# Kernel tuning notes

Hardware: AMD Instinct MI355X
Metric: run time of the kernel (lower is better)

## Reference

```python
import jax, jax.numpy as jnp
import numpy as np


def setup_inputs() -> dict:
    key = jax.random.key(0)
    ks = jax.random.split(key, 5)
    B, Lq, Lk, KD, E, VD = 2, 1024, 1024, 128, 128, 128
    return {
        "query": jax.random.normal(ks[0], (B, Lq, KD), dtype=jnp.float32),
        "key": jax.random.normal(ks[1], (B, Lk, KD), dtype=jnp.float32),
        "value": jax.random.normal(ks[2], (B, Lk, VD), dtype=jnp.float32),
        "vT": jax.random.normal(ks[3], (E,), dtype=jnp.float32) * (1.0 / np.sqrt(E)),
        "weight": jax.random.normal(ks[4], (E, 2 * KD), dtype=jnp.float32) * (1.0 / np.sqrt(2 * KD)),
    }


def reference(query, key, value, vT, weight):
    # Additive (Bahdanau) attention: score(i,j) = vT . tanh(W @ concat(q_i, k_j))
    kdim = query.shape[-1]
    Wq = weight[:, :kdim]   # [E, kdim] acts on query half of concat
    Wk = weight[:, kdim:]   # [E, kdim] acts on key half
    qp = jnp.einsum("bqd,ed->bqe", query, Wq)   # [B, Lq, E]
    kp = jnp.einsum("bkd,ed->bke", key, Wk)     # [B, Lk, E]
    # broadcast-add replaces the explicit concat+linear: [B, Lq, Lk, E]
    h = jnp.tanh(qp[:, :, None, :] + kp[:, None, :, :])
    scores = jnp.einsum("bqke,e->bqk", h, vT)    # [B, Lq, Lk]
    attn = jax.nn.softmax(scores, axis=-1)
    return jnp.einsum("bqk,bkv->bqv", attn, value)  # [B, Lq, Vd]
```

## Files before the change

### kernel.cpp

```cpp
#include <hip/hip_runtime.h>

#define CSC 2.88539008177792681f

typedef float v2f __attribute__((ext_vector_type(2)));

__device__ __forceinline__ float fast_exp2(float x) {
  return __builtin_amdgcn_exp2f(x);
}
__device__ __forceinline__ float fast_rcp(float x) {
  return __builtin_amdgcn_rcpf(x);
}
__device__ __forceinline__ v2f vfma(v2f a, v2f b, v2f c) {
  return __builtin_elementwise_fma(a, b, c);
}
__device__ __forceinline__ v2f vsplat(float s) {
  v2f r;
  r[0] = s;
  r[1] = s;
  return r;
}

__global__ __launch_bounds__(256) void proj_kernel(
    const float* __restrict__ query, const float* __restrict__ key,
    const float* __restrict__ weight, float* __restrict__ Eq,
    float* __restrict__ EkT) {
  __shared__ __align__(16) float rows[16][128];
  __shared__ __align__(16) float tile[16][128];
  int blk = blockIdx.x;
  bool isK = blk >= 128;
  const float* src = isK ? key : query;
  int woff = isK ? 128 : 0;
  int row0 = (isK ? blk - 128 : blk) * 16;
  int tid = threadIdx.x;
#pragma unroll
  for (int i = 0; i < 8; ++i) {
    int f = i * 256 + tid;
    rows[f >> 7][f & 127] = src[(size_t)row0 * 128 + f];
  }
  __syncthreads();
  int e = tid & 127;
  int rh = (tid >> 7) * 8;
  float acc[8];
#pragma unroll
  for (int i = 0; i < 8; ++i) acc[i] = 0.f;
  const float4* wrow =
      reinterpret_cast<const float4*>(weight + (size_t)e * 256 + woff);
#pragma unroll 4
  for (int d4 = 0; d4 < 32; ++d4) {
    float4 wv = wrow[d4];
#pragma unroll
    for (int i = 0; i < 8; ++i) {
      float4 rv = *reinterpret_cast<const float4*>(&rows[rh + i][d4 * 4]);
      acc[i] = fmaf(rv.x, wv.x, acc[i]);
      acc[i] = fmaf(rv.y, wv.y, acc[i]);
      acc[i] = fmaf(rv.z, wv.z, acc[i]);
      acc[i] = fmaf(rv.w, wv.w, acc[i]);
    }
  }
  if (!isK) {
#pragma unroll
    for (int i = 0; i < 8; ++i)
      Eq[(size_t)(row0 + rh + i) * 128 + e] = fast_exp2(CSC * acc[i]);
  } else {
#pragma unroll
    for (int i = 0; i < 8; ++i) tile[rh + i][e] = fast_exp2(CSC * acc[i]);
    __syncthreads();
    int eo = tid >> 1;
    int rseg = (tid & 1) * 8;
    float4 v0 = make_float4(tile[rseg + 0][eo], tile[rseg + 1][eo],
                            tile[rseg + 2][eo], tile[rseg + 3][eo]);
    float4 v1 = make_float4(tile[rseg + 4][eo], tile[rseg + 5][eo],
                            tile[rseg + 6][eo], tile[rseg + 7][eo]);
    float* dst = EkT + (size_t)eo * 2048 + row0 + rseg;
    *reinterpret_cast<float4*>(dst) = v0;
    *reinterpret_cast<float4*>(dst + 4) = v1;
  }
}

__device__ __forceinline__ void quad4(const float4 eq, const float4 vt, v2f ek0,
                                      v2f ek1, v2f ek2, v2f ek3, v2f& acc) {
  v2f one = vsplat(1.f);
  v2f A0 = vfma(vsplat(eq.x), ek0, one);
  v2f A1 = vfma(vsplat(eq.y), ek1, one);
  v2f A2 = vfma(vsplat(eq.z), ek2, one);
  v2f A3 = vfma(vsplat(eq.w), ek3, one);
  v2f P01 = A0 * A1;
  v2f P23 = A2 * A3;
  v2f t01 = vfma(vsplat(vt.x), A1, vsplat(vt.y) * A0);
  v2f t23 = vfma(vsplat(vt.z), A3, vsplat(vt.w) * A2);
  v2f num = vfma(t23, P01, t01 * P23);
  v2f den = P01 * P23;
  v2f r;
  r[0] = fast_rcp(den[0]);
  r[1] = fast_rcp(den[1]);
  acc = vfma(num, r, acc);
}

__global__ __launch_bounds__(1024, 4) void attn_kernel(
    const float* __restrict__ Eq, const float* __restrict__ EkT,
    const float* __restrict__ vT, const float* __restrict__ value,
    float* __restrict__ out) {
  __shared__ __align__(16) float sc[8][1024];
  __shared__ __align__(16) v2f pout[16][8][64];
  __shared__ float wsum[16][4];
  __shared__ float denom[8];

  int tid = threadIdx.x;
  int lane = tid & 63;
  int w = tid >> 6;
  int b = blockIdx.x >> 7;
  int q0 = (blockIdx.x & 127) * 8;
  int half = tid >> 9;
  int kp = tid & 511;
  int qh = half * 4;

  {
    const float* ekp = EkT + (size_t)b * 1024 + 2 * kp;
    const float* eqb = Eq + (size_t)(b * 1024 + q0 + qh) * 128;
    v2f acc[4];
#pragma unroll
    for (int q = 0; q < 4; ++q) acc[q] = vsplat(0.f);
#pragma unroll 2
    for (int e = 0; e < 128; e += 4) {
      v2f ek0 = *reinterpret_cast<const v2f*>(ekp + (size_t)(e + 0) * 2048);
      v2f ek1 = *reinterpret_cast<const v2f*>(ekp + (size_t)(e + 1) * 2048);
      v2f ek2 = *reinterpret_cast<const v2f*>(ekp + (size_t)(e + 2) * 2048);
      v2f ek3 = *reinterpret_cast<const v2f*>(ekp + (size_t)(e + 3) * 2048);
      float4 vt4 = *reinterpret_cast<const float4*>(vT + e);
#pragma unroll
      for (int q = 0; q < 4; ++q) {
        float4 eq4 =
            *reinterpret_cast<const float4*>(eqb + (size_t)q * 128 + e);
        quad4(eq4, vt4, ek0, ek1, ek2, ek3, acc[q]);
      }
    }
#pragma unroll
    for (int q = 0; q < 4; ++q) {
      v2f p;
      p[0] = fast_exp2(-CSC * acc[q][0]);
      p[1] = fast_exp2(-CSC * acc[q][1]);
      *reinterpret_cast<v2f*>(&sc[qh + q][2 * kp]) = p;
      float s = p[0] + p[1];
#pragma unroll
      for (int off = 32; off; off >>= 1) s += __shfl_xor(s, off);
      if (lane == 0) wsum[w][q] = s;
    }
  }
  __syncthreads();
  if (tid < 8) {
    int base = (tid >> 2) * 8;
    float s = 0.f;
#pragma unroll
    for (int ww = 0; ww < 8; ++ww) s += wsum[base + ww][tid & 3];
    denom[tid] = s;
  }

  {
    int kb = w * 64;
    v2f acc2[8];
#pragma unroll
    for (int q = 0; q < 8; ++q) acc2[q] = vsplat(0.f);
    const v2f* vp =
        reinterpret_cast<const v2f*>(value) + (size_t)b * 1024 * 64 + lane;
#pragma unroll 2
    for (int kk = 0; kk < 64; kk += 4) {
      v2f vv0 = vp[(size_t)(kb + kk + 0) * 64];
      v2f vv1 = vp[(size_t)(kb + kk + 1) * 64];
      v2f vv2 = vp[(size_t)(kb + kk + 2) * 64];
      v2f vv3 = vp[(size_t)(kb + kk + 3) * 64];
#pragma unroll
      for (int q = 0; q < 8; ++q) {
        float4 pp = *reinterpret_cast<const float4*>(&sc[q][kb + kk]);
        acc2[q] = vfma(vsplat(pp.x), vv0, acc2[q]);
        acc2[q] = vfma(vsplat(pp.y), vv1, acc2[q]);
        acc2[q] = vfma(vsplat(pp.z), vv2, acc2[q]);
        acc2[q] = vfma(vsplat(pp.w), vv3, acc2[q]);
      }
    }
#pragma unroll
    for (int q = 0; q < 8; ++q) pout[w][q][lane] = acc2[q];
  }
  __syncthreads();

  if (tid < 512) {
    int q = tid >> 6;
    v2f r = pout[0][q][lane];
#pragma unroll
    for (int ww = 1; ww < 16; ++ww) r = r + pout[ww][q][lane];
    float inv = fast_rcp(denom[q]);
    r[0] *= inv;
    r[1] *= inv;
    reinterpret_cast<v2f*>(out)[(size_t)(b * 1024 + q0 + q) * 64 + lane] = r;
  }
}

extern "C" void kernel_launch(void* const* d_in, const int* in_sizes, int n_in,
                              void* d_out, int out_size, void* d_ws,
                              size_t ws_size, hipStream_t stream) {
  const float* query = (const float*)d_in[0];
  const float* key = (const float*)d_in[1];
  const float* value = (const float*)d_in[2];
  const float* vT = (const float*)d_in[3];
  const float* weight = (const float*)d_in[4];
  float* out = (float*)d_out;
  float* Eq = (float*)d_ws;
  float* EkT = Eq + 2048 * 128;
  proj_kernel<<<256, 256, 0, stream>>>(query, key, weight, Eq, EkT);
  attn_kernel<<<256, 1024, 0, stream>>>(Eq, EkT, vT, value, out);
}
```

Baseline: 55.44 us.

## Store key projections in e4-interleaved layout and give each thread one key over eight queries

The proj kernel now writes the exponentiated key projections in a layout where four consecutive E-values of a key sit together as a float4, using a padded shared tile. The score loop has each thread handle one key and all eight queries with scalar math, replacing two keys times four queries with packed v2f math. This means one float4 load feeds eight queries and the query loads are warp-uniform. The final reduction now uses all 1024 threads, each writing one scalar output. The risk is losing packed-FMA throughput and raising register pressure from eight scalar accumulators.

```diff
diff --git a/kernel.cpp b/kernel.cpp
--- a/kernel.cpp
+++ b/kernel.cpp
@@ -23,9 +23,9 @@
 __global__ __launch_bounds__(256) void proj_kernel(
     const float* __restrict__ query, const float* __restrict__ key,
     const float* __restrict__ weight, float* __restrict__ Eq,
-    float* __restrict__ EkT) {
+    float* __restrict__ EkT4) {
   __shared__ __align__(16) float rows[16][128];
-  __shared__ __align__(16) float tile[16][128];
+  __shared__ __align__(16) float tile[16][132];
   int blk = blockIdx.x;
   bool isK = blk >= 128;
   const float* src = isK ? key : query;
@@ -65,44 +65,25 @@
 #pragma unroll
     for (int i = 0; i < 8; ++i) tile[rh + i][e] = fast_exp2(CSC * acc[i]);
     __syncthreads();
-    int eo = tid >> 1;
-    int rseg = (tid & 1) * 8;
-    float4 v0 = make_float4(tile[rseg + 0][eo], tile[rseg + 1][eo],
-                            tile[rseg + 2][eo], tile[rseg + 3][eo]);
-    float4 v1 = make_float4(tile[rseg + 4][eo], tile[rseg + 5][eo],
-                            tile[rseg + 6][eo], tile[rseg + 7][eo]);
-    float* dst = EkT + (size_t)eo * 2048 + row0 + rseg;
-    *reinterpret_cast<float4*>(dst) = v0;
-    *reinterpret_cast<float4*>(dst + 4) = v1;
+    int kk = tid & 15;
+    int e4a = tid >> 4;
+#pragma unroll
+    for (int h = 0; h < 2; ++h) {
+      int ee = e4a + h * 16;
+      float4 v = *reinterpret_cast<const float4*>(&tile[kk][ee * 4]);
+      *reinterpret_cast<float4*>(EkT4 + ((size_t)ee * 2048 + row0 + kk) * 4) =
+          v;
+    }
   }
 }
 
-__device__ __forceinline__ void quad4(const float4 eq, const float4 vt, v2f ek0,
-                                      v2f ek1, v2f ek2, v2f ek3, v2f& acc) {
-  v2f one = vsplat(1.f);
-  v2f A0 = vfma(vsplat(eq.x), ek0, one);
-  v2f A1 = vfma(vsplat(eq.y), ek1, one);
-  v2f A2 = vfma(vsplat(eq.z), ek2, one);
-  v2f A3 = vfma(vsplat(eq.w), ek3, one);
-  v2f P01 = A0 * A1;
-  v2f P23 = A2 * A3;
-  v2f t01 = vfma(vsplat(vt.x), A1, vsplat(vt.y) * A0);
-  v2f t23 = vfma(vsplat(vt.z), A3, vsplat(vt.w) * A2);
-  v2f num = vfma(t23, P01, t01 * P23);
-  v2f den = P01 * P23;
-  v2f r;
-  r[0] = fast_rcp(den[0]);
-  r[1] = fast_rcp(den[1]);
-  acc = vfma(num, r, acc);
-}
-
 __global__ __launch_bounds__(1024, 4) void attn_kernel(
-    const float* __restrict__ Eq, const float* __restrict__ EkT,
+    const float* __restrict__ Eq, const float* __restrict__ EkT4,
     const float* __restrict__ vT, const float* __restrict__ value,
     float* __restrict__ out) {
   __shared__ __align__(16) float sc[8][1024];
-  __shared__ __align__(16) v2f pout[16][8][64];
-  __shared__ float wsum[16][4];
+  __shared__ __align__(16) float pout[16][8][128];
+  __shared__ float wsum[16][8];
   __shared__ float denom[8];
 
   int tid = threadIdx.x;
@@ -110,37 +91,39 @@
   int w = tid >> 6;
   int b = blockIdx.x >> 7;
   int q0 = (blockIdx.x & 127) * 8;
-  int half = tid >> 9;
-  int kp = tid & 511;
-  int qh = half * 4;
 
   {
-    const float* ekp = EkT + (size_t)b * 1024 + 2 * kp;
-    const float* eqb = Eq + (size_t)(b * 1024 + q0 + qh) * 128;
-    v2f acc[4];
+    const float4* ekp =
+        reinterpret_cast<const float4*>(EkT4) + (size_t)b * 1024 + tid;
+    const float* eqb = Eq + (size_t)(b * 1024 + q0) * 128;
+    const float4* vtp = reinterpret_cast<const float4*>(vT);
+    float acc[8];
 #pragma unroll
-    for (int q = 0; q < 4; ++q) acc[q] = vsplat(0.f);
-#pragma unroll 2
-    for (int e = 0; e < 128; e += 4) {
-      v2f ek0 = *reinterpret_cast<const v2f*>(ekp + (size_t)(e + 0) * 2048);
-      v2f ek1 = *reinterpret_cast<const v2f*>(ekp + (size_t)(e + 1) * 2048);
-      v2f ek2 = *reinterpret_cast<const v2f*>(ekp + (size_t)(e + 2) * 2048);
-      v2f ek3 = *reinterpret_cast<const v2f*>(ekp + (size_t)(e + 3) * 2048);
-      float4 vt4 = *reinterpret_cast<const float4*>(vT + e);
+    for (int q = 0; q < 8; ++q) acc[q] = 0.f;
+    for (int e4 = 0; e4 < 32; ++e4) {
+      float4 ek = ekp[(size_t)e4 * 2048];
+      float4 vt4 = vtp[e4];
 #pragma unroll
-      for (int q = 0; q < 4; ++q) {
-        float4 eq4 =
-            *reinterpret_cast<const float4*>(eqb + (size_t)q * 128 + e);
-        quad4(eq4, vt4, ek0, ek1, ek2, ek3, acc[q]);
+      for (int q = 0; q < 8; ++q) {
+        float4 eqq = *reinterpret_cast<const float4*>(
+            eqb + (size_t)q * 128 + e4 * 4);
+        float A0 = fmaf(eqq.x, ek.x, 1.f);
+        float A1 = fmaf(eqq.y, ek.y, 1.f);
+        float A2 = fmaf(eqq.z, ek.z, 1.f);
+        float A3 = fmaf(eqq.w, ek.w, 1.f);
+        float P01 = A0 * A1;
+        float P23 = A2 * A3;
+        float t01 = fmaf(vt4.x, A1, vt4.y * A0);
+        float t23 = fmaf(vt4.z, A3, vt4.w * A2);
+        float num = fmaf(t23, P01, t01 * P23);
+        acc[q] = fmaf(num, fast_rcp(P01 * P23), acc[q]);
       }
     }
 #pragma unroll
-    for (int q = 0; q < 4; ++q) {
-      v2f p;
-      p[0] = fast_exp2(-CSC * acc[q][0]);
-      p[1] = fast_exp2(-CSC * acc[q][1]);
-      *reinterpret_cast<v2f*>(&sc[qh + q][2 * kp]) = p;
-      float s = p[0] + p[1];
+    for (int q = 0; q < 8; ++q) {
+      float p = fast_exp2(-CSC * acc[q]);
+      sc[q][tid] = p;
+      float s = p;
 #pragma unroll
       for (int off = 32; off; off >>= 1) s += __shfl_xor(s, off);
       if (lane == 0) wsum[w][q] = s;
@@ -148,10 +131,9 @@
   }
   __syncthreads();
   if (tid < 8) {
-    int base = (tid >> 2) * 8;
     float s = 0.f;
 #pragma unroll
-    for (int ww = 0; ww < 8; ++ww) s += wsum[base + ww][tid & 3];
+    for (int ww = 0; ww < 16; ++ww) s += wsum[ww][tid];
     denom[tid] = s;
   }
 
@@ -160,17 +142,17 @@
     v2f acc2[8];
 #pragma unroll
     for (int q = 0; q < 8; ++q) acc2[q] = vsplat(0.f);
-    const v2f* vp =
-        reinterpret_cast<const v2f*>(value) + (size_t)b * 1024 * 64 + lane;
+    const v2f* vp = reinterpret_cast<const v2f*>(value) +
+                    ((size_t)b * 1024 + kb) * 64 + lane;
 #pragma unroll 2
-    for (int kk = 0; kk < 64; kk += 4) {
-      v2f vv0 = vp[(size_t)(kb + kk + 0) * 64];
-      v2f vv1 = vp[(size_t)(kb + kk + 1) * 64];
-      v2f vv2 = vp[(size_t)(kb + kk + 2) * 64];
-      v2f vv3 = vp[(size_t)(kb + kk + 3) * 64];
+    for (int k4 = 0; k4 < 16; ++k4) {
+      v2f vv0 = vp[(size_t)(k4 * 4 + 0) * 64];
+      v2f vv1 = vp[(size_t)(k4 * 4 + 1) * 64];
+      v2f vv2 = vp[(size_t)(k4 * 4 + 2) * 64];
+      v2f vv3 = vp[(size_t)(k4 * 4 + 3) * 64];
 #pragma unroll
       for (int q = 0; q < 8; ++q) {
-        float4 pp = *reinterpret_cast<const float4*>(&sc[q][kb + kk]);
+        float4 pp = *reinterpret_cast<const float4*>(&sc[q][kb + k4 * 4]);
         acc2[q] = vfma(vsplat(pp.x), vv0, acc2[q]);
         acc2[q] = vfma(vsplat(pp.y), vv1, acc2[q]);
         acc2[q] = vfma(vsplat(pp.z), vv2, acc2[q]);
@@ -178,19 +160,19 @@
       }
     }
 #pragma unroll
-    for (int q = 0; q < 8; ++q) pout[w][q][lane] = acc2[q];
+    for (int q = 0; q < 8; ++q)
+      *reinterpret_cast<v2f*>(&pout[w][q][2 * lane]) = acc2[q];
   }
   __syncthreads();
 
-  if (tid < 512) {
-    int q = tid >> 6;
-    v2f r = pout[0][q][lane];
+  {
+    int q = tid >> 7;
+    int c = tid & 127;
+    float r = 0.f;
 #pragma unroll
-    for (int ww = 1; ww < 16; ++ww) r = r + pout[ww][q][lane];
-    float inv = fast_rcp(denom[q]);
-    r[0] *= inv;
-    r[1] *= inv;
-    reinterpret_cast<v2f*>(out)[(size_t)(b * 1024 + q0 + q) * 64 + lane] = r;
+    for (int ww = 0; ww < 16; ++ww) r += pout[ww][q][c];
+    r *= fast_rcp(denom[q]);
+    out[((size_t)b * 1024 + q0 + q) * 128 + c] = r;
   }
 }
 
@@ -204,7 +186,7 @@
   const float* weight = (const float*)d_in[4];
   float* out = (float*)d_out;
   float* Eq = (float*)d_ws;
-  float* EkT = Eq + 2048 * 128;
-  proj_kernel<<<256, 256, 0, stream>>>(query, key, weight, Eq, EkT);
-  attn_kernel<<<256, 1024, 0, stream>>>(Eq, EkT, vT, value, out);
+  float* EkT4 = Eq + 262144;
+  proj_kernel<<<256, 256, 0, stream>>>(query, key, weight, Eq, EkT4);
+  attn_kernel<<<256, 1024, 0, stream>>>(Eq, EkT4, vT, value, out);
 }
```

Result: faster. 50.28 us (-9.3%).
